# Performance work log

Measured on AMD Instinct MI355X. Metric: run time of the kernel, lower is better.

The kernel has to match this reference:

```python
import jax, jax.numpy as jnp
import numpy as np

CLIP_LIMIT = 10.0
NTILES = 8        # OpenCV createCLAHE default tileGridSize=(8,8)
NBINS = 256

_M_RGB2XYZ = jnp.array([[0.412453, 0.357580, 0.180423],
                        [0.212671, 0.715160, 0.072169],
                        [0.019334, 0.119193, 0.950227]], dtype=jnp.float32)
_M_XYZ2RGB = jnp.array([[ 3.240479, -1.537150, -0.498535],
                        [-0.969256,  1.875992,  0.041556],
                        [ 0.055648, -0.204043,  1.057311]], dtype=jnp.float32)
_WP = jnp.array([0.950456, 1.0, 1.088754], dtype=jnp.float32)  # D65 white point (OpenCV)
_EPS = 0.008856


def rgb2lab(rgb):  # rgb: [H,W,3] in [0,1]
    xyz = jnp.einsum('hwc,dc->hwd', rgb, _M_RGB2XYZ) / _WP
    f = jnp.where(xyz > _EPS, jnp.cbrt(xyz), 7.787 * xyz + 16.0 / 116.0)
    fx, fy, fz = f[..., 0], f[..., 1], f[..., 2]
    L = 116.0 * fy - 16.0
    a = 500.0 * (fx - fy)
    b = 200.0 * (fy - fz)
    return L, a, b


def lab2rgb(L, a, b):
    fy = (L + 16.0) / 116.0
    fx = fy + a / 500.0
    fz = fy - b / 200.0
    f = jnp.stack([fx, fy, fz], axis=-1)
    xyz = jnp.where(f ** 3 > _EPS, f ** 3, (f - 16.0 / 116.0) / 7.787) * _WP
    rgb = jnp.einsum('hwd,cd->hwc', xyz, _M_XYZ2RGB)
    return jnp.clip(rgb, 0.0, 1.0)


def clahe_channel(L8, clip_limit):
    # L8: [H,W] int32 in [0,255]
    H, W = L8.shape
    th, tw = H // NTILES, W // NTILES
    area = float(th * tw)
    # per-tile histograms via one scatter-add
    rows = jnp.arange(H) // th            # [H] tile row id
    cols = jnp.arange(W) // tw            # [W] tile col id
    tid = rows[:, None] * NTILES + cols[None, :]          # [H,W]
    flat = (tid * NBINS + L8).ravel()
    hist = jnp.zeros(NTILES * NTILES * NBINS, jnp.float32).at[flat].add(1.0)
    hist = hist.reshape(NTILES * NTILES, NBINS)
    # clip + uniform redistribution of excess
    clip = max(clip_limit * area / NBINS, 1.0)
    excess = jnp.sum(jnp.maximum(hist - clip, 0.0), axis=1, keepdims=True)
    hist = jnp.minimum(hist, clip) + excess / NBINS
    # CDF -> LUT (OpenCV: lutScale = 255/tileArea, rounded)
    cdf = jnp.cumsum(hist, axis=1)
    lut = jnp.clip(jnp.round(cdf * (255.0 / area)), 0.0, 255.0)  # [T, 256]
    # bilinear interpolation between tile LUTs
    fy = jnp.clip((jnp.arange(H, dtype=jnp.float32) + 0.5) / th - 0.5, 0.0, NTILES - 1.0)
    fx = jnp.clip((jnp.arange(W, dtype=jnp.float32) + 0.5) / tw - 0.5, 0.0, NTILES - 1.0)
    y0 = jnp.floor(fy).astype(jnp.int32); y1 = jnp.minimum(y0 + 1, NTILES - 1)
    x0 = jnp.floor(fx).astype(jnp.int32); x1 = jnp.minimum(x0 + 1, NTILES - 1)
    wy = (fy - y0)[:, None]; wx = (fx - x0)[None, :]
    def g(yi, xi):  # gather LUT value for each pixel from tile (yi, xi)
        return lut[yi[:, None] * NTILES + xi[None, :], L8]
    top = (1.0 - wx) * g(y0, x0) + wx * g(y0, x1)
    bot = (1.0 - wx) * g(y1, x0) + wx * g(y1, x1)
    return (1.0 - wy) * top + wy * bot   # [H,W] float in [0,255]


def setup_inputs() -> dict:
    key = jax.random.key(0)
    x = jax.random.uniform(key, (3, 2048, 2048), dtype=jnp.float32)
    return {"x": x}


def reference(x) -> jnp.ndarray:
    hwc = jnp.transpose(x, (1, 2, 0))          # CHW -> HWC
    L, a, b = rgb2lab(hwc)                      # L in [0,100]
    L8 = jnp.clip(jnp.round(L * (255.0 / 100.0)), 0, 255).astype(jnp.int32)
    L_eq = clahe_channel(L8, CLIP_LIMIT) * (100.0 / 255.0)
    rgb = lab2rgb(L_eq, a, b)
    return jnp.transpose(rgb, (2, 0, 1))        # HWC -> CHW
```

## Files before the change

### kernel.cpp

```cpp
#include <hip/hip_runtime.h>
#include <stdint.h>

#define HW 4194304
#define WIDTH 2048
#define NBLK 2048
#define F(x) ((float)(x))

__device__ __forceinline__ float cbrtf_glibc(float x) {
    unsigned int bits = __float_as_uint(x);
    int xe = (int)((bits >> 23) & 0xFF) - 126;
    float xm = __uint_as_float((bits & 0x007FFFFFu) | 0x3F000000u);

    double xmd = (double)xm;
    double p = __dsub_rn(0.697570460207922770, __dmul_rn(0.191502161678719066, xmd));
    p = __dadd_rn(0.492659620528969547, __dmul_rn(p, xmd));
    float u = (float)p;

    float t2 = __fmul_rn(__fmul_rn(u, u), u);

    double ud  = (double)u;
    double t2d = (double)t2;
    double num = __dmul_rn(ud, __dadd_rn(t2d, __dmul_rn(2.0, xmd)));
    double den = __dadd_rn(__dmul_rn(2.0, t2d), xmd);

    int idx = 2 + (xe % 3);
    double f = (idx == 2) ? 1.0
             : (idx == 0) ? (1.0 / 1.5874010519681994748)
             : (idx == 1) ? (1.0 / 1.2599210498948731648)
             : (idx == 3) ? 1.2599210498948731648
             :              1.5874010519681994748;
    double ym  = __dmul_rn(__ddiv_rn(num, den), f);
    float ymf = (float)ym;

    int q = xe / 3;
    float s = (q == 0) ? 1.0f : ((q == -1) ? 0.5f : 0.25f);
    return __fmul_rn(ymf, s);
}

__device__ __forceinline__ void rgb2lab_px(float r, float g, float b,
                                           int& l8, float& A_, float& B_) {
    float X = __fadd_rn(__fadd_rn(__fmul_rn(r, F(0.412453)), __fmul_rn(g, F(0.357580))), __fmul_rn(b, F(0.180423)));
    float Y = __fadd_rn(__fadd_rn(__fmul_rn(r, F(0.212671)), __fmul_rn(g, F(0.715160))), __fmul_rn(b, F(0.072169)));
    float Z = __fadd_rn(__fadd_rn(__fmul_rn(r, F(0.019334)), __fmul_rn(g, F(0.119193))), __fmul_rn(b, F(0.950227)));
    X = __fdiv_rn(X, F(0.950456));
    Z = __fdiv_rn(Z, F(1.088754));
    const float EPS = F(0.008856);
    const float C0  = F(16.0 / 116.0);
    float fx = (X > EPS) ? cbrtf_glibc(X) : __fadd_rn(__fmul_rn(F(7.787), X), C0);
    float fy = (Y > EPS) ? cbrtf_glibc(Y) : __fadd_rn(__fmul_rn(F(7.787), Y), C0);
    float fz = (Z > EPS) ? cbrtf_glibc(Z) : __fadd_rn(__fmul_rn(F(7.787), Z), C0);
    float L  = __fsub_rn(__fmul_rn(F(116.0), fy), F(16.0));
    A_ = __fmul_rn(F(500.0), __fsub_rn(fx, fy));
    B_ = __fmul_rn(F(200.0), __fsub_rn(fy, fz));
    float Lr = rintf(__fmul_rn(L, F(255.0 / 100.0)));
    Lr = fminf(fmaxf(Lr, 0.0f), 255.0f);
    l8 = (int)Lr;
}

__device__ __forceinline__ void lab2rgb_px(float Leq, float A_, float B_,
                                           float& rr, float& gg, float& bb) {
    const float EPS = F(0.008856);
    const float C0  = F(16.0 / 116.0);
    float fy2 = __fdiv_rn(__fadd_rn(Leq, 16.0f), 116.0f);
    float fx2 = __fadd_rn(fy2, __fdiv_rn(A_, 500.0f));
    float fz2 = __fsub_rn(fy2, __fdiv_rn(B_, 200.0f));
    float t3;
    t3 = fx2 * fx2 * fx2;
    float X = ((t3 > EPS) ? t3 : __fdiv_rn(__fsub_rn(fx2, C0), F(7.787))) * F(0.950456);
    t3 = fy2 * fy2 * fy2;
    float Y = ((t3 > EPS) ? t3 : __fdiv_rn(__fsub_rn(fy2, C0), F(7.787))) * F(1.0);
    t3 = fz2 * fz2 * fz2;
    float Z = ((t3 > EPS) ? t3 : __fdiv_rn(__fsub_rn(fz2, C0), F(7.787))) * F(1.088754);
    rr = __fadd_rn(__fadd_rn(__fmul_rn(X, F(3.240479)),  __fmul_rn(Y, F(-1.537150))), __fmul_rn(Z, F(-0.498535)));
    gg = __fadd_rn(__fadd_rn(__fmul_rn(X, F(-0.969256)), __fmul_rn(Y, F(1.875992))),  __fmul_rn(Z, F(0.041556)));
    bb = __fadd_rn(__fadd_rn(__fmul_rn(X, F(0.055648)),  __fmul_rn(Y, F(-0.204043))), __fmul_rn(Z, F(1.057311)));
    rr = fminf(fmaxf(rr, 0.0f), 1.0f);
    gg = fminf(fmaxf(gg, 0.0f), 1.0f);
    bb = fminf(fmaxf(bb, 0.0f), 1.0f);
}

template<bool ATOMIC_LOADS>
__device__ __forceinline__ void build_luts(const unsigned int* __restrict__ hist,
                                           float* lutS, int y0, int y1, int t) {
    const int lane = t & 63;
    const int w = t >> 6;
    #pragma unroll
    for (int i = 0; i < 4; ++i) {
        int gidx = w * 4 + i;
        int trow = gidx >> 3;
        int tcol = gidx & 7;
        int tile = (trow ? y1 : y0) * 8 + tcol;
        float h0, h1, h2, h3;
        if (ATOMIC_LOADS) {
            const unsigned int* hp = hist + tile * 256 + lane * 4;
            h0 = (float)__hip_atomic_load(&hp[0], __ATOMIC_RELAXED, __HIP_MEMORY_SCOPE_AGENT);
            h1 = (float)__hip_atomic_load(&hp[1], __ATOMIC_RELAXED, __HIP_MEMORY_SCOPE_AGENT);
            h2 = (float)__hip_atomic_load(&hp[2], __ATOMIC_RELAXED, __HIP_MEMORY_SCOPE_AGENT);
            h3 = (float)__hip_atomic_load(&hp[3], __ATOMIC_RELAXED, __HIP_MEMORY_SCOPE_AGENT);
        } else {
            uint4 hv = *(const uint4*)(hist + tile * 256 + lane * 4);
            h0 = (float)hv.x; h1 = (float)hv.y; h2 = (float)hv.z; h3 = (float)hv.w;
        }
        float e = __fadd_rn(__fadd_rn(fmaxf(h0 - 2560.0f, 0.0f),
                                      fmaxf(h1 - 2560.0f, 0.0f)),
                            __fadd_rn(fmaxf(h2 - 2560.0f, 0.0f),
                                      fmaxf(h3 - 2560.0f, 0.0f)));
        #pragma unroll
        for (int d = 1; d < 64; d <<= 1) e = __fadd_rn(e, __shfl_xor(e, d));
        float ex = __fmul_rn(e, F(1.0 / 256.0));
        float v0 = __fadd_rn(fminf(h0, 2560.0f), ex);
        float v1 = __fadd_rn(fminf(h1, 2560.0f), ex);
        float v2 = __fadd_rn(fminf(h2, 2560.0f), ex);
        float v3 = __fadd_rn(fminf(h3, 2560.0f), ex);
        float s0 = v0;
        float s1 = __fadd_rn(s0, v1);
        float s2 = __fadd_rn(s1, v2);
        float s3 = __fadd_rn(s2, v3);
        float sc = s3;
        #pragma unroll
        for (int d = 1; d < 64; d <<= 1) {
            float u2 = __shfl_up(sc, d);
            if (lane >= d) sc = __fadd_rn(sc, u2);
        }
        float excl = __fsub_rn(sc, s3);
        int lb = trow * 2048 + tcol * 256 + lane * 4;
        float c0 = rintf(__fmul_rn(__fadd_rn(excl, s0), F(255.0 / 65536.0)));
        float c1 = rintf(__fmul_rn(__fadd_rn(excl, s1), F(255.0 / 65536.0)));
        float c2 = rintf(__fmul_rn(__fadd_rn(excl, s2), F(255.0 / 65536.0)));
        float c3 = rintf(__fmul_rn(__fadd_rn(excl, s3), F(255.0 / 65536.0)));
        lutS[lb + 0] = fminf(fmaxf(c0, 0.0f), 255.0f);
        lutS[lb + 1] = fminf(fmaxf(c1, 0.0f), 255.0f);
        lutS[lb + 2] = fminf(fmaxf(c2, 0.0f), 255.0f);
        lutS[lb + 3] = fminf(fmaxf(c3, 0.0f), 255.0f);
    }
}

__device__ __forceinline__ void apply4(const float* lutS, int col0, int idx,
        int l80, int l81, int l82, int l83,
        float A0, float A1, float A2, float A3,
        float B0, float B1, float B2, float B3,
        float wy, float omwy, float* __restrict__ out) {
    float4 o_r, o_g, o_b;
#define PIX(J, L8V, AV, BV, OR_, OG_, OB_) {                                      \
    int col = col0 + (J);                                                         \
    float fxc = fminf(fmaxf(((float)col + 0.5f) * (1.0f / 256.0f) - 0.5f, 0.0f), 7.0f); \
    int xi0 = (int)floorf(fxc);                                                   \
    int xi1 = min(xi0 + 1, 7);                                                    \
    float wx = __fsub_rn(fxc, (float)xi0);                                        \
    float omwx = __fsub_rn(1.0f, wx);                                             \
    float g00 = lutS[xi0 * 256 + (L8V)];                                          \
    float g01 = lutS[xi1 * 256 + (L8V)];                                          \
    float g10 = lutS[2048 + xi0 * 256 + (L8V)];                                   \
    float g11 = lutS[2048 + xi1 * 256 + (L8V)];                                   \
    float top_ = __fadd_rn(__fmul_rn(omwx, g00), __fmul_rn(wx, g01));             \
    float bot_ = __fadd_rn(__fmul_rn(omwx, g10), __fmul_rn(wx, g11));             \
    float Leq = __fmul_rn(__fadd_rn(__fmul_rn(omwy, top_), __fmul_rn(wy, bot_)),  \
                          F(100.0 / 255.0));                                      \
    lab2rgb_px(Leq, (AV), (BV), (OR_), (OG_), (OB_));                             \
}
    PIX(0, l80, A0, B0, o_r.x, o_g.x, o_b.x);
    PIX(1, l81, A1, B1, o_r.y, o_g.y, o_b.y);
    PIX(2, l82, A2, B2, o_r.z, o_g.z, o_b.z);
    PIX(3, l83, A3, B3, o_r.w, o_g.w, o_b.w);
#undef PIX
    *(float4*)(out + idx)          = o_r;
    *(float4*)(out + idx + HW)     = o_g;
    *(float4*)(out + idx + 2 * HW) = o_b;
}

__global__ __launch_bounds__(256, 8) void k_fused_reg(const float* __restrict__ x,
        unsigned int* __restrict__ hist, unsigned int* __restrict__ rowdone,
        float* __restrict__ out) {
    __shared__ float lutS[4096];
    unsigned int* h = (unsigned int*)lutS;
    const int t = threadIdx.x;
    const int y = blockIdx.x;

    #pragma unroll
    for (int i = 0; i < 8; ++i) h[i * 256 + t] = 0;
    __syncthreads();

    const int rowbase = y * WIDTH;

    float A0, A1, A2, A3, A4, A5, A6, A7;
    float B0, B1, B2, B3, B4, B5, B6, B7;
    unsigned pk0, pk1;
    {
        const int col0 = 4 * t;
        const int idx  = rowbase + col0;
        float4 r4 = *(const float4*)(x + idx);
        float4 g4 = *(const float4*)(x + idx + HW);
        float4 b4 = *(const float4*)(x + idx + 2 * HW);
        int l0, l1, l2, l3;
        rgb2lab_px(r4.x, g4.x, b4.x, l0, A0, B0);
        rgb2lab_px(r4.y, g4.y, b4.y, l1, A1, B1);
        rgb2lab_px(r4.z, g4.z, b4.z, l2, A2, B2);
        rgb2lab_px(r4.w, g4.w, b4.w, l3, A3, B3);
        const int hb = (col0 >> 8) << 8;
        atomicAdd(&h[hb + l0], 1u);
        atomicAdd(&h[hb + l1], 1u);
        atomicAdd(&h[hb + l2], 1u);
        atomicAdd(&h[hb + l3], 1u);
        pk0 = (unsigned)l0 | ((unsigned)l1 << 8) | ((unsigned)l2 << 16) | ((unsigned)l3 << 24);
    }
    {
        const int col0 = 1024 + 4 * t;
        const int idx  = rowbase + col0;
        float4 r4 = *(const float4*)(x + idx);
        float4 g4 = *(const float4*)(x + idx + HW);
        float4 b4 = *(const float4*)(x + idx + 2 * HW);
        int l0, l1, l2, l3;
        rgb2lab_px(r4.x, g4.x, b4.x, l0, A4, B4);
        rgb2lab_px(r4.y, g4.y, b4.y, l1, A5, B5);
        rgb2lab_px(r4.z, g4.z, b4.z, l2, A6, B6);
        rgb2lab_px(r4.w, g4.w, b4.w, l3, A7, B7);
        const int hb = (col0 >> 8) << 8;
        atomicAdd(&h[hb + l0], 1u);
        atomicAdd(&h[hb + l1], 1u);
        atomicAdd(&h[hb + l2], 1u);
        atomicAdd(&h[hb + l3], 1u);
        pk1 = (unsigned)l0 | ((unsigned)l1 << 8) | ((unsigned)l2 << 16) | ((unsigned)l3 << 24);
    }
    __syncthreads();
    {
        unsigned int* gh = hist + (y >> 8) * 2048;
        #pragma unroll
        for (int i = 0; i < 8; ++i) {
            unsigned int v = h[i * 256 + t];
            if (v) atomicAdd(&gh[i * 256 + t], v);
        }
    }
    __syncthreads();

    float fyc = fminf(fmaxf(((float)y + 0.5f) * (1.0f / 256.0f) - 0.5f, 0.0f), 7.0f);
    int y0 = (int)floorf(fyc);
    int y1 = min(y0 + 1, 7);
    float wy = __fsub_rn(fyc, (float)y0);
    float omwy = __fsub_rn(1.0f, wy);

    if (t == 0) {
        __threadfence();
        atomicAdd(&rowdone[y >> 8], 1u);
        long limit = 1L << 18;
        while (limit-- > 0) {
            unsigned a = __hip_atomic_load(&rowdone[y0], __ATOMIC_ACQUIRE, __HIP_MEMORY_SCOPE_AGENT);
            unsigned b = __hip_atomic_load(&rowdone[y1], __ATOMIC_ACQUIRE, __HIP_MEMORY_SCOPE_AGENT);
            if (a == 256u && b == 256u) break;
            __builtin_amdgcn_s_sleep(2);
        }
    }
    __syncthreads();

    build_luts<true>(hist, lutS, y0, y1, t);
    __syncthreads();

    apply4(lutS, 4 * t, rowbase + 4 * t,
           (int)(pk0 & 0xFFu), (int)((pk0 >> 8) & 0xFFu),
           (int)((pk0 >> 16) & 0xFFu), (int)((pk0 >> 24) & 0xFFu),
           A0, A1, A2, A3, B0, B1, B2, B3, wy, omwy, out);
    apply4(lutS, 1024 + 4 * t, rowbase + 1024 + 4 * t,
           (int)(pk1 & 0xFFu), (int)((pk1 >> 8) & 0xFFu),
           (int)((pk1 >> 16) & 0xFFu), (int)((pk1 >> 24) & 0xFFu),
           A4, A5, A6, A7, B4, B5, B6, B7, wy, omwy, out);
}

__global__ __launch_bounds__(256, 8) void k_fused_ws(const float* __restrict__ x,
        unsigned int* __restrict__ hist, unsigned int* __restrict__ rowdone,
        float* __restrict__ Abuf, float* __restrict__ Bbuf,
        unsigned int* __restrict__ l8buf, float* __restrict__ out) {
    __shared__ float lutS[4096];
    unsigned int* h = (unsigned int*)lutS;
    const int t = threadIdx.x;
    const int y = blockIdx.x;

    #pragma unroll
    for (int i = 0; i < 8; ++i) h[i * 256 + t] = 0;
    __syncthreads();

    const int rowbase = y * WIDTH;
    #pragma unroll
    for (int ch = 0; ch < 2; ++ch) {
        const int col0 = ch * 1024 + 4 * t;
        const int idx  = rowbase + col0;
        float4 r4 = *(const float4*)(x + idx);
        float4 g4 = *(const float4*)(x + idx + HW);
        float4 b4 = *(const float4*)(x + idx + 2 * HW);
        int l80, l81, l82, l83;
        float A0, A1, A2, A3, B0, B1, B2, B3;
        rgb2lab_px(r4.x, g4.x, b4.x, l80, A0, B0);
        rgb2lab_px(r4.y, g4.y, b4.y, l81, A1, B1);
        rgb2lab_px(r4.z, g4.z, b4.z, l82, A2, B2);
        rgb2lab_px(r4.w, g4.w, b4.w, l83, A3, B3);
        const int hb = (col0 >> 8) << 8;
        atomicAdd(&h[hb + l80], 1u);
        atomicAdd(&h[hb + l81], 1u);
        atomicAdd(&h[hb + l82], 1u);
        atomicAdd(&h[hb + l83], 1u);
        *(float4*)(Abuf + idx) = make_float4(A0, A1, A2, A3);
        *(float4*)(Bbuf + idx) = make_float4(B0, B1, B2, B3);
        l8buf[idx >> 2] = (unsigned)l80 | ((unsigned)l81 << 8)
                        | ((unsigned)l82 << 16) | ((unsigned)l83 << 24);
    }
    __syncthreads();
    {
        unsigned int* gh = hist + (y >> 8) * 2048;
        #pragma unroll
        for (int i = 0; i < 8; ++i) {
            unsigned int v = h[i * 256 + t];
            if (v) atomicAdd(&gh[i * 256 + t], v);
        }
    }
    __syncthreads();

    float fyc = fminf(fmaxf(((float)y + 0.5f) * (1.0f / 256.0f) - 0.5f, 0.0f), 7.0f);
    int y0 = (int)floorf(fyc);
    int y1 = min(y0 + 1, 7);
    float wy = __fsub_rn(fyc, (float)y0);
    float omwy = __fsub_rn(1.0f, wy);

    if (t == 0) {
        __threadfence();
        atomicAdd(&rowdone[y >> 8], 1u);
        long limit = 1L << 18;
        while (limit-- > 0) {
            unsigned a = __hip_atomic_load(&rowdone[y0], __ATOMIC_ACQUIRE, __HIP_MEMORY_SCOPE_AGENT);
            unsigned b = __hip_atomic_load(&rowdone[y1], __ATOMIC_ACQUIRE, __HIP_MEMORY_SCOPE_AGENT);
            if (a == 256u && b == 256u) break;
            __builtin_amdgcn_s_sleep(2);
        }
    }
    __syncthreads();

    build_luts<true>(hist, lutS, y0, y1, t);
    __syncthreads();

    #pragma unroll
    for (int ch = 0; ch < 2; ++ch) {
        const int col0 = ch * 1024 + 4 * t;
        const int idx  = rowbase + col0;
        float4 a4 = *(const float4*)(Abuf + idx);
        float4 b4 = *(const float4*)(Bbuf + idx);
        unsigned p = l8buf[idx >> 2];
        apply4(lutS, col0, idx,
               (int)(p & 0xFFu), (int)((p >> 8) & 0xFFu),
               (int)((p >> 16) & 0xFFu), (int)((p >> 24) & 0xFFu),
               a4.x, a4.y, a4.z, a4.w, b4.x, b4.y, b4.z, b4.w,
               wy, omwy, out);
    }
}

__global__ __launch_bounds__(256, 8) void k_hist_ab(const float* __restrict__ x,
        unsigned int* __restrict__ hist,
        float* __restrict__ Abuf, float* __restrict__ Bbuf,
        unsigned int* __restrict__ l8buf, int store) {
    __shared__ unsigned int h[2048];
    const int t = threadIdx.x;
    const int y = blockIdx.x;
    #pragma unroll
    for (int i = 0; i < 8; ++i) h[i * 256 + t] = 0;
    __syncthreads();

    const int rowbase = y * WIDTH;
    #pragma unroll
    for (int ch = 0; ch < 2; ++ch) {
        const int col0 = ch * 1024 + 4 * t;
        const int idx  = rowbase + col0;
        float4 r4 = *(const float4*)(x + idx);
        float4 g4 = *(const float4*)(x + idx + HW);
        float4 b4 = *(const float4*)(x + idx + 2 * HW);
        int l80, l81, l82, l83;
        float A0, A1, A2, A3, B0, B1, B2, B3;
        rgb2lab_px(r4.x, g4.x, b4.x, l80, A0, B0);
        rgb2lab_px(r4.y, g4.y, b4.y, l81, A1, B1);
        rgb2lab_px(r4.z, g4.z, b4.z, l82, A2, B2);
        rgb2lab_px(r4.w, g4.w, b4.w, l83, A3, B3);
        const int hb = (col0 >> 8) << 8;
        atomicAdd(&h[hb + l80], 1u);
        atomicAdd(&h[hb + l81], 1u);
        atomicAdd(&h[hb + l82], 1u);
        atomicAdd(&h[hb + l83], 1u);
        if (store) {
            *(float4*)(Abuf + idx) = make_float4(A0, A1, A2, A3);
            *(float4*)(Bbuf + idx) = make_float4(B0, B1, B2, B3);
            l8buf[idx >> 2] = (unsigned)l80 | ((unsigned)l81 << 8)
                            | ((unsigned)l82 << 16) | ((unsigned)l83 << 24);
        }
    }
    __syncthreads();
    unsigned int* gh = hist + (y >> 8) * 2048;
    #pragma unroll
    for (int i = 0; i < 8; ++i) {
        unsigned int v = h[i * 256 + t];
        if (v) atomicAdd(&gh[i * 256 + t], v);
    }
}

__global__ __launch_bounds__(256, 8) void k_lut_apply(const float* __restrict__ x,
        const unsigned int* __restrict__ hist,
        const float* __restrict__ Abuf, const float* __restrict__ Bbuf,
        const unsigned int* __restrict__ l8buf,
        float* __restrict__ out, int stored) {
    __shared__ float lutS[4096];
    const int t = threadIdx.x;
    const int y = blockIdx.x;

    float fyc = fminf(fmaxf(((float)y + 0.5f) * (1.0f / 256.0f) - 0.5f, 0.0f), 7.0f);
    int y0 = (int)floorf(fyc);
    int y1 = min(y0 + 1, 7);
    float wy = __fsub_rn(fyc, (float)y0);
    float omwy = __fsub_rn(1.0f, wy);

    build_luts<false>(hist, lutS, y0, y1, t);
    __syncthreads();

    const int rowbase = y * WIDTH;
    #pragma unroll
    for (int ch = 0; ch < 2; ++ch) {
        const int col0 = ch * 1024 + 4 * t;
        const int idx  = rowbase + col0;
        float A0, A1, A2, A3, B0, B1, B2, B3;
        int l80, l81, l82, l83;
        if (stored) {
            float4 a4 = *(const float4*)(Abuf + idx);
            float4 b4 = *(const float4*)(Bbuf + idx);
            unsigned p = l8buf[idx >> 2];
            A0 = a4.x; A1 = a4.y; A2 = a4.z; A3 = a4.w;
            B0 = b4.x; B1 = b4.y; B2 = b4.z; B3 = b4.w;
            l80 = (int)(p & 0xFFu); l81 = (int)((p >> 8) & 0xFFu);
            l82 = (int)((p >> 16) & 0xFFu); l83 = (int)((p >> 24) & 0xFFu);
        } else {
            float4 r4 = *(const float4*)(x + idx);
            float4 g4 = *(const float4*)(x + idx + HW);
            float4 b4 = *(const float4*)(x + idx + 2 * HW);
            rgb2lab_px(r4.x, g4.x, b4.x, l80, A0, B0);
            rgb2lab_px(r4.y, g4.y, b4.y, l81, A1, B1);
            rgb2lab_px(r4.z, g4.z, b4.z, l82, A2, B2);
            rgb2lab_px(r4.w, g4.w, b4.w, l83, A3, B3);
        }
        apply4(lutS, col0, idx, l80, l81, l82, l83,
               A0, A1, A2, A3, B0, B1, B2, B3, wy, omwy, out);
    }
}

extern "C" void kernel_launch(void* const* d_in, const int* in_sizes, int n_in,
                              void* d_out, int out_size, void* d_ws, size_t ws_size,
                              hipStream_t stream) {
    const float* x = (const float*)d_in[0];
    float* out = (float*)d_out;
    char* ws = (char*)d_ws;
    unsigned int* hist = (unsigned int*)ws;
    unsigned int* rowdone = (unsigned int*)(ws + 65536);
    const size_t off = 131072;
    float* Abuf = (float*)(ws + off);
    float* Bbuf = (float*)(ws + off + (size_t)HW * 4);
    unsigned int* l8buf = (unsigned int*)(ws + off + (size_t)HW * 8);
    const size_t need = off + (size_t)HW * 9;
    const int store = (ws_size >= need) ? 1 : 0;

    static int mode = -1;
    if (mode < 0) {
        int ncu = 0, dev = 0;
        (void)hipGetDevice(&dev);
        (void)hipDeviceGetAttribute(&ncu, hipDeviceAttributeMultiprocessorCount, dev);
        int nbR = 0, nbW = 0;
        bool occR = (hipOccupancyMaxActiveBlocksPerMultiprocessor(&nbR, k_fused_reg, 256, 0) == hipSuccess)
                    && (nbR * ncu >= NBLK);
        bool occW = (hipOccupancyMaxActiveBlocksPerMultiprocessor(&nbW, k_fused_ws, 256, 0) == hipSuccess)
                    && (nbW * ncu >= NBLK);
        hipFuncAttributes fa{};
        bool nospill = (hipFuncGetAttributes(&fa, (const void*)k_fused_reg) == hipSuccess)
                       && (fa.localSizeBytes == 0);
        if (occR && nospill)            mode = 0;
        else if (occW && store == 1)    mode = 1;
        else                            mode = 2;
    }

    (void)hipMemsetAsync(ws, 0, 65536 + 64, stream);

    if (mode == 0) {
        k_fused_reg<<<NBLK, 256, 0, stream>>>(x, hist, rowdone, out);
    } else if (mode == 1) {
        k_fused_ws<<<NBLK, 256, 0, stream>>>(x, hist, rowdone, Abuf, Bbuf, l8buf, out);
    } else {
        k_hist_ab<<<NBLK, 256, 0, stream>>>(x, hist, Abuf, Bbuf, l8buf, store);
        k_lut_apply<<<NBLK, 256, 0, stream>>>(x, hist, Abuf, Bbuf, l8buf, out, store);
    }
}
```

Before: 128.3 us.

## Add half-register fused kernel variant and sched barriers to cut register pressure

Adds sched_barrier fences inside the per-chunk Lab conversion so the compiler cannot interleave all eight pixels, which lowers peak register use in the register-resident fused kernel. Also adds a hybrid fused kernel that keeps half the row's a/b/L8 values in registers and spills the other half to workspace. It is picked when the fully register-resident kernel cannot fit all blocks co-resident or spills. The barriers may reduce instruction-level parallelism, and the hybrid path adds extra global traffic for the spilled half.

New measurement: 128.2 us. No clear change (-0.1%).

```diff
diff --git a/kernel.cpp b/kernel.cpp
--- a/kernel.cpp
+++ b/kernel.cpp
@@ -168,6 +168,45 @@
     *(float4*)(out + idx + 2 * HW) = o_b;
 }
 
+__device__ __forceinline__ void chunk_lab(const float* __restrict__ x,
+        unsigned int* h, int rowbase, int col0,
+        float& A0, float& A1, float& A2, float& A3,
+        float& B0, float& B1, float& B2, float& B3, unsigned& pk) {
+    const int idx = rowbase + col0;
+    float4 r4 = *(const float4*)(x + idx);
+    float4 g4 = *(const float4*)(x + idx + HW);
+    float4 b4 = *(const float4*)(x + idx + 2 * HW);
+    int l0, l1, l2, l3;
+    rgb2lab_px(r4.x, g4.x, b4.x, l0, A0, B0);
+    rgb2lab_px(r4.y, g4.y, b4.y, l1, A1, B1);
+    __builtin_amdgcn_sched_barrier(0);
+    rgb2lab_px(r4.z, g4.z, b4.z, l2, A2, B2);
+    rgb2lab_px(r4.w, g4.w, b4.w, l3, A3, B3);
+    __builtin_amdgcn_sched_barrier(0);
+    const int hb = (col0 >> 8) << 8;
+    atomicAdd(&h[hb + l0], 1u);
+    atomicAdd(&h[hb + l1], 1u);
+    atomicAdd(&h[hb + l2], 1u);
+    atomicAdd(&h[hb + l3], 1u);
+    pk = (unsigned)l0 | ((unsigned)l1 << 8) | ((unsigned)l2 << 16) | ((unsigned)l3 << 24);
+}
+
+__device__ __forceinline__ void signal_and_wait(unsigned int* rowdone,
+                                                int myrow, int y0, int y1, int t) {
+    if (t == 0) {
+        __threadfence();
+        atomicAdd(&rowdone[myrow], 1u);
+        long limit = 1L << 18;
+        while (limit-- > 0) {
+            unsigned a = __hip_atomic_load(&rowdone[y0], __ATOMIC_ACQUIRE, __HIP_MEMORY_SCOPE_AGENT);
+            unsigned b = __hip_atomic_load(&rowdone[y1], __ATOMIC_ACQUIRE, __HIP_MEMORY_SCOPE_AGENT);
+            if (a == 256u && b == 256u) break;
+            __builtin_amdgcn_s_sleep(2);
+        }
+    }
+    __syncthreads();
+}
+
 __global__ __launch_bounds__(256, 8) void k_fused_reg(const float* __restrict__ x,
         unsigned int* __restrict__ hist, unsigned int* __restrict__ rowdone,
         float* __restrict__ out) {
@@ -181,46 +220,13 @@
     __syncthreads();
 
     const int rowbase = y * WIDTH;
-
     float A0, A1, A2, A3, A4, A5, A6, A7;
     float B0, B1, B2, B3, B4, B5, B6, B7;
     unsigned pk0, pk1;
-    {
-        const int col0 = 4 * t;
-        const int idx  = rowbase + col0;
-        float4 r4 = *(const float4*)(x + idx);
-        float4 g4 = *(const float4*)(x + idx + HW);
-        float4 b4 = *(const float4*)(x + idx + 2 * HW);
-        int l0, l1, l2, l3;
-        rgb2lab_px(r4.x, g4.x, b4.x, l0, A0, B0);
-        rgb2lab_px(r4.y, g4.y, b4.y, l1, A1, B1);
-        rgb2lab_px(r4.z, g4.z, b4.z, l2, A2, B2);
-        rgb2lab_px(r4.w, g4.w, b4.w, l3, A3, B3);
-        const int hb = (col0 >> 8) << 8;
-        atomicAdd(&h[hb + l0], 1u);
-        atomicAdd(&h[hb + l1], 1u);
-        atomicAdd(&h[hb + l2], 1u);
-        atomicAdd(&h[hb + l3], 1u);
-        pk0 = (unsigned)l0 | ((unsigned)l1 << 8) | ((unsigned)l2 << 16) | ((unsigned)l3 << 24);
-    }
-    {
-        const int col0 = 1024 + 4 * t;
-        const int idx  = rowbase + col0;
-        float4 r4 = *(const float4*)(x + idx);
-        float4 g4 = *(const float4*)(x + idx + HW);
-        float4 b4 = *(const float4*)(x + idx + 2 * HW);
-        int l0, l1, l2, l3;
-        rgb2lab_px(r4.x, g4.x, b4.x, l0, A4, B4);
-        rgb2lab_px(r4.y, g4.y, b4.y, l1, A5, B5);
-        rgb2lab_px(r4.z, g4.z, b4.z, l2, A6, B6);
-        rgb2lab_px(r4.w, g4.w, b4.w, l3, A7, B7);
-        const int hb = (col0 >> 8) << 8;
-        atomicAdd(&h[hb + l0], 1u);
-        atomicAdd(&h[hb + l1], 1u);
-        atomicAdd(&h[hb + l2], 1u);
-        atomicAdd(&h[hb + l3], 1u);
-        pk1 = (unsigned)l0 | ((unsigned)l1 << 8) | ((unsigned)l2 << 16) | ((unsigned)l3 << 24);
-    }
+    chunk_lab(x, h, rowbase, 4 * t,        A0, A1, A2, A3, B0, B1, B2, B3, pk0);
+    __builtin_amdgcn_sched_barrier(0);
+    chunk_lab(x, h, rowbase, 1024 + 4 * t, A4, A5, A6, A7, B4, B5, B6, B7, pk1);
+    __builtin_amdgcn_sched_barrier(0);
     __syncthreads();
     {
         unsigned int* gh = hist + (y >> 8) * 2048;
@@ -238,18 +244,7 @@
     float wy = __fsub_rn(fyc, (float)y0);
     float omwy = __fsub_rn(1.0f, wy);
 
-    if (t == 0) {
-        __threadfence();
-        atomicAdd(&rowdone[y >> 8], 1u);
-        long limit = 1L << 18;
-        while (limit-- > 0) {
-            unsigned a = __hip_atomic_load(&rowdone[y0], __ATOMIC_ACQUIRE, __HIP_MEMORY_SCOPE_AGENT);
-            unsigned b = __hip_atomic_load(&rowdone[y1], __ATOMIC_ACQUIRE, __HIP_MEMORY_SCOPE_AGENT);
-            if (a == 256u && b == 256u) break;
-            __builtin_amdgcn_s_sleep(2);
-        }
-    }
-    __syncthreads();
+    signal_and_wait(rowdone, y >> 8, y0, y1, t);
 
     build_luts<true>(hist, lutS, y0, y1, t);
     __syncthreads();
@@ -262,6 +257,75 @@
            (int)(pk1 & 0xFFu), (int)((pk1 >> 8) & 0xFFu),
            (int)((pk1 >> 16) & 0xFFu), (int)((pk1 >> 24) & 0xFFu),
            A4, A5, A6, A7, B4, B5, B6, B7, wy, omwy, out);
+}
+
+__global__ __launch_bounds__(256, 8) void k_fused_half(const float* __restrict__ x,
+        unsigned int* __restrict__ hist, unsigned int* __restrict__ rowdone,
+        float* __restrict__ Abuf, float* __restrict__ Bbuf,
+        unsigned int* __restrict__ l8buf, float* __restrict__ out) {
+    __shared__ float lutS[4096];
+    unsigned int* h = (unsigned int*)lutS;
+    const int t = threadIdx.x;
+    const int y = blockIdx.x;
+
+    #pragma unroll
+    for (int i = 0; i < 8; ++i) h[i * 256 + t] = 0;
+    __syncthreads();
+
+    const int rowbase = y * WIDTH;
+    float A0, A1, A2, A3, B0, B1, B2, B3;
+    unsigned pk0;
+    chunk_lab(x, h, rowbase, 4 * t, A0, A1, A2, A3, B0, B1, B2, B3, pk0);
+    __builtin_amdgcn_sched_barrier(0);
+    {
+        float Aa, Ab, Ac, Ad, Ba, Bb, Bc, Bd;
+        unsigned pk1;
+        const int col0 = 1024 + 4 * t;
+        const int idx  = rowbase + col0;
+        chunk_lab(x, h, rowbase, col0, Aa, Ab, Ac, Ad, Ba, Bb, Bc, Bd, pk1);
+        *(float4*)(Abuf + idx) = make_float4(Aa, Ab, Ac, Ad);
+        *(float4*)(Bbuf + idx) = make_float4(Ba, Bb, Bc, Bd);
+        l8buf[idx >> 2] = pk1;
+    }
+    __builtin_amdgcn_sched_barrier(0);
+    __syncthreads();
+    {
+        unsigned int* gh = hist + (y >> 8) * 2048;
+        #pragma unroll
+        for (int i = 0; i < 8; ++i) {
+            unsigned int v = h[i * 256 + t];
+            if (v) atomicAdd(&gh[i * 256 + t], v);
+        }
+    }
+    __syncthreads();
+
+    float fyc = fminf(fmaxf(((float)y + 0.5f) * (1.0f / 256.0f) - 0.5f, 0.0f), 7.0f);
+    int y0 = (int)floorf(fyc);
+    int y1 = min(y0 + 1, 7);
+    float wy = __fsub_rn(fyc, (float)y0);
+    float omwy = __fsub_rn(1.0f, wy);
+
+    signal_and_wait(rowdone, y >> 8, y0, y1, t);
+
+    build_luts<true>(hist, lutS, y0, y1, t);
+    __syncthreads();
+
+    apply4(lutS, 4 * t, rowbase + 4 * t,
+           (int)(pk0 & 0xFFu), (int)((pk0 >> 8) & 0xFFu),
+           (int)((pk0 >> 16) & 0xFFu), (int)((pk0 >> 24) & 0xFFu),
+           A0, A1, A2, A3, B0, B1, B2, B3, wy, omwy, out);
+    {
+        const int col0 = 1024 + 4 * t;
+        const int idx  = rowbase + col0;
+        float4 a4 = *(const float4*)(Abuf + idx);
+        float4 b4 = *(const float4*)(Bbuf + idx);
+        unsigned p = l8buf[idx >> 2];
+        apply4(lutS, col0, idx,
+               (int)(p & 0xFFu), (int)((p >> 8) & 0xFFu),
+               (int)((p >> 16) & 0xFFu), (int)((p >> 24) & 0xFFu),
+               a4.x, a4.y, a4.z, a4.w, b4.x, b4.y, b4.z, b4.w,
+               wy, omwy, out);
+    }
 }
 
 __global__ __launch_bounds__(256, 8) void k_fused_ws(const float* __restrict__ x,
@@ -318,18 +382,7 @@
     float wy = __fsub_rn(fyc, (float)y0);
     float omwy = __fsub_rn(1.0f, wy);
 
-    if (t == 0) {
-        __threadfence();
-        atomicAdd(&rowdone[y >> 8], 1u);
-        long limit = 1L << 18;
-        while (limit-- > 0) {
-            unsigned a = __hip_atomic_load(&rowdone[y0], __ATOMIC_ACQUIRE, __HIP_MEMORY_SCOPE_AGENT);
-            unsigned b = __hip_atomic_load(&rowdone[y1], __ATOMIC_ACQUIRE, __HIP_MEMORY_SCOPE_AGENT);
-            if (a == 256u && b == 256u) break;
-            __builtin_amdgcn_s_sleep(2);
-        }
-    }
-    __syncthreads();
+    signal_and_wait(rowdone, y >> 8, y0, y1, t);
 
     build_luts<true>(hist, lutS, y0, y1, t);
     __syncthreads();
@@ -462,17 +515,24 @@
         int ncu = 0, dev = 0;
         (void)hipGetDevice(&dev);
         (void)hipDeviceGetAttribute(&ncu, hipDeviceAttributeMultiprocessorCount, dev);
-        int nbR = 0, nbW = 0;
-        bool occR = (hipOccupancyMaxActiveBlocksPerMultiprocessor(&nbR, k_fused_reg, 256, 0) == hipSuccess)
-                    && (nbR * ncu >= NBLK);
-        bool occW = (hipOccupancyMaxActiveBlocksPerMultiprocessor(&nbW, k_fused_ws, 256, 0) == hipSuccess)
-                    && (nbW * ncu >= NBLK);
+        int nb = 0;
         hipFuncAttributes fa{};
-        bool nospill = (hipFuncGetAttributes(&fa, (const void*)k_fused_reg) == hipSuccess)
-                       && (fa.localSizeBytes == 0);
-        if (occR && nospill)            mode = 0;
-        else if (occW && store == 1)    mode = 1;
-        else                            mode = 2;
+        bool okReg = (hipOccupancyMaxActiveBlocksPerMultiprocessor(&nb, k_fused_reg, 256, 0) == hipSuccess)
+                     && (nb * ncu >= NBLK)
+                     && (hipFuncGetAttributes(&fa, (const void*)k_fused_reg) == hipSuccess)
+                     && (fa.localSizeBytes == 0);
+        nb = 0; fa = hipFuncAttributes{};
+        bool okHalf = (hipOccupancyMaxActiveBlocksPerMultiprocessor(&nb, k_fused_half, 256, 0) == hipSuccess)
+                      && (nb * ncu >= NBLK)
+                      && (hipFuncGetAttributes(&fa, (const void*)k_fused_half) == hipSuccess)
+                      && (fa.localSizeBytes == 0);
+        nb = 0;
+        bool okWs = (hipOccupancyMaxActiveBlocksPerMultiprocessor(&nb, k_fused_ws, 256, 0) == hipSuccess)
+                    && (nb * ncu >= NBLK);
+        if (okReg)                       mode = 0;
+        else if (okHalf && store == 1)   mode = 1;
+        else if (okWs && store == 1)     mode = 2;
+        else                             mode = 3;
     }
 
     (void)hipMemsetAsync(ws, 0, 65536 + 64, stream);
@@ -480,6 +540,8 @@
     if (mode == 0) {
         k_fused_reg<<<NBLK, 256, 0, stream>>>(x, hist, rowdone, out);
     } else if (mode == 1) {
+        k_fused_half<<<NBLK, 256, 0, stream>>>(x, hist, rowdone, Abuf, Bbuf, l8buf, out);
+    } else if (mode == 2) {
         k_fused_ws<<<NBLK, 256, 0, stream>>>(x, hist, rowdone, Abuf, Bbuf, l8buf, out);
     } else {
         k_hist_ab<<<NBLK, 256, 0, stream>>>(x, hist, Abuf, Bbuf, l8buf, store);
```
